# Performance work log

Measured on AMD Instinct MI355X. Metric: run time of the kernel, lower is better.

Reference implementation:

```python
import jax, jax.numpy as jnp
import numpy as np

NUM_CAPSULE = 16
DIM_CAPSULE = 64
ROUTINGS = 3
T_EPS = 1e-07


def squash(v, axis=-1):
    # NOTE: this repo's 'squash' is v / sqrt(||v||^2 + eps) (norm-only scaling)
    s = jnp.sum(v * v, axis=axis, keepdims=True)
    return v / jnp.sqrt(s + T_EPS)


def setup_inputs() -> dict:
    key = jax.random.key(0)
    k1, k2 = jax.random.split(key)
    B, N_in, D_in = 64, 512, 1024
    x = jax.random.normal(k1, (B, N_in, D_in), dtype=jnp.float32)
    # xavier-normal-ish init for W [1, D_in, num_capsule*dim_capsule]
    fan_in, fan_out = D_in, NUM_CAPSULE * DIM_CAPSULE
    std = float(np.sqrt(2.0 / (fan_in + fan_out)))
    W = jax.random.normal(k2, (1, D_in, NUM_CAPSULE * DIM_CAPSULE), dtype=jnp.float32) * std
    return {"x": x, "W": W}


def reference(x, W):
    B, N_in, D_in = x.shape
    # u_hat: [B, N_in, num_cap*dim_cap] -> [B, num_cap, N_in, dim_cap]
    u_hat = jnp.matmul(x, W[0])
    u_hat = u_hat.reshape(B, N_in, NUM_CAPSULE, DIM_CAPSULE).transpose(0, 2, 1, 3)
    b = jnp.zeros((B, NUM_CAPSULE, N_in), dtype=u_hat.dtype)
    outputs = None
    for i in range(ROUTINGS):
        # torch code permutes to [B, N_in, num_cap], softmaxes dim=2, permutes back:
        # equivalent to softmax over the num_capsule axis (axis=1)
        c = jax.nn.softmax(b, axis=1)  # [B, num_cap, N_in]
        outputs = squash(jnp.einsum('bij,bijk->bik', c, u_hat))  # [B, num_cap, dim_cap]
        if i < ROUTINGS - 1:
            b = jnp.einsum('bik,bijk->bij', outputs, u_hat)  # [B, num_cap, N_in]
    return outputs
```

## Files before the change

kernel.cpp:

```cpp
#include <hip/hip_runtime.h>
#include <stdint.h>

#define NUM_CAP 16
#define DIM_CAP 64
#define BATCH   64
#define N_IN    512
#define D_IN    1024
#define N_COL   1024
#define M_ROWS  (BATCH*N_IN)

typedef __attribute__((ext_vector_type(8))) short short8;
typedef __attribute__((ext_vector_type(4))) float f32x4;

__device__ __forceinline__ float bf2f(unsigned int u) {
  return __uint_as_float(u << 16);
}
__device__ __forceinline__ unsigned short f2bf_rne(float f) {
  unsigned int x = __float_as_uint(f);
  x += 0x7fffu + ((x >> 16) & 1u);
  return (unsigned short)(x >> 16);
}
__device__ __forceinline__ unsigned int pack_rne(unsigned int lo, unsigned int hi) {
  const unsigned int lr = lo + (0x7fffu + ((lo >> 16) & 1u));
  const unsigned int hr = hi + (0x7fffu + ((hi >> 16) & 1u));
  return (lr >> 16) | (hr & 0xffff0000u);
}

__global__ __launch_bounds__(256) void prep(
    const float* __restrict__ x, const float* __restrict__ W,
    unsigned short* __restrict__ xb, unsigned short* __restrict__ Wt) {
  const int t = threadIdx.x;
  if (blockIdx.x < 16384) {
    const size_t i = ((size_t)blockIdx.x * 256 + t) * 8;
    const uint4 a = *(const uint4*)(x + i);
    const uint4 b = *(const uint4*)(x + i + 4);
    uint4 p;
    p.x = pack_rne(a.x, a.y); p.y = pack_rne(a.z, a.w);
    p.z = pack_rne(b.x, b.y); p.w = pack_rne(b.z, b.w);
    *(uint4*)(xb + i) = p;
  } else {
    __shared__ float tile[32][33];
    const int bid = blockIdx.x - 16384;
    const int bx = bid & 31, by = bid >> 5;
    const int tx = t & 31, ty0 = t >> 5;
    #pragma unroll
    for (int r = 0; r < 4; r++) {
      const int ty = ty0 + r * 8;
      tile[ty][tx] = W[(size_t)(by * 32 + ty) * N_COL + bx * 32 + tx];
    }
    __syncthreads();
    #pragma unroll
    for (int r = 0; r < 4; r++) {
      const int ty = ty0 + r * 8;
      Wt[(size_t)(bx * 32 + ty) * D_IN + by * 32 + tx] = f2bf_rne(tile[tx][ty]);
    }
  }
}

__global__ __launch_bounds__(256) void gemm_uhat(
    const unsigned short* __restrict__ A,
    const unsigned short* __restrict__ Bt,
    unsigned short* __restrict__ C,
    float* __restrict__ Pp) {
  __shared__ __align__(16) unsigned short lA[128 * 32];
  __shared__ __align__(16) unsigned short lB[128 * 32];
  __shared__ float cs2[2][128];

  const int t = threadIdx.x;
  const int wave = t >> 6, lane = t & 63;
  const int xcd = blockIdx.x & 7, local = blockIdx.x >> 3;
  const int mt = xcd * 32 + (local >> 3), nt = local & 7;
  const int m0 = mt * 128, n0 = nt * 128;
  const int wm = wave & 1, wn = wave >> 1;

  f32x4 acc[4][4] = {};

  const int srow = lane >> 2;
  const int schunk = ((lane & 3) ^ ((srow >> 1) & 3)) * 8;

  for (int kt = 0; kt < D_IN / 32; ++kt) {
    const int k0 = kt * 32;
    __syncthreads();
    #pragma unroll
    for (int s0 = 0; s0 < 2; ++s0) {
      const int s = wave + s0 * 4;
      const unsigned short* ga = A + (size_t)(m0 + s * 16 + srow) * D_IN + k0 + schunk;
      __builtin_amdgcn_global_load_lds(
          (const __attribute__((address_space(1))) void*)ga,
          (__attribute__((address_space(3))) void*)(lA + s * 512), 16, 0, 0);
      const unsigned short* gb = Bt + (size_t)(n0 + s * 16 + srow) * D_IN + k0 + schunk;
      __builtin_amdgcn_global_load_lds(
          (const __attribute__((address_space(1))) void*)gb,
          (__attribute__((address_space(3))) void*)(lB + s * 512), 16, 0, 0);
    }
    __syncthreads();

    short8 af[4], bfr[4];
    const int rsel = lane & 15;
    const int q = lane >> 4;
    const int koff = (q ^ ((rsel >> 1) & 3)) * 8;
    #pragma unroll
    for (int tm = 0; tm < 4; tm++)
      af[tm] = *(const short8*)&lA[(wm * 64 + tm * 16 + rsel) * 32 + koff];
    #pragma unroll
    for (int tn = 0; tn < 4; tn++)
      bfr[tn] = *(const short8*)&lB[(wn * 64 + tn * 16 + rsel) * 32 + koff];
    #pragma unroll
    for (int tm = 0; tm < 4; tm++)
      #pragma unroll
      for (int tn = 0; tn < 4; tn++)
        acc[tm][tn] = __builtin_amdgcn_mfma_f32_16x16x32_bf16(
            af[tm], bfr[tn], acc[tm][tn], 0, 0, 0);
  }

  const int lrow = (lane >> 4) * 4, lcol = lane & 15;
  #pragma unroll
  for (int tm = 0; tm < 4; tm++)
    #pragma unroll
    for (int tn = 0; tn < 4; tn++)
      #pragma unroll
      for (int r = 0; r < 4; r++) {
        const int row = m0 + wm * 64 + tm * 16 + lrow + r;
        const int col = n0 + wn * 64 + tn * 16 + lcol;
        C[(size_t)row * N_COL + col] = f2bf_rne(acc[tm][tn][r]);
      }

  #pragma unroll
  for (int tn = 0; tn < 4; tn++) {
    float p = 0.f;
    #pragma unroll
    for (int tm = 0; tm < 4; tm++)
      #pragma unroll
      for (int r = 0; r < 4; r++) p += acc[tm][tn][r];
    p += __shfl_xor(p, 16);
    p += __shfl_xor(p, 32);
    if (lane < 16) cs2[wm][wn * 64 + tn * 16 + lane] = p;
  }
  __syncthreads();
  if (t < 128)
    Pp[(size_t)mt * N_COL + n0 + t] = cs2[0][t] + cs2[1][t];
}

__global__ __launch_bounds__(256) void k_v(
    const float* __restrict__ Pin, float* __restrict__ vout, const int nstrips) {
  const int b = blockIdx.x, t = threadIdx.x;
  float4 s = make_float4(0.f, 0.f, 0.f, 0.f);
  for (int q = 0; q < nstrips; ++q) {
    const float4 p = *(const float4*)&Pin[((size_t)b * nstrips + q) * 1024 + t * 4];
    s.x += p.x; s.y += p.y; s.z += p.z; s.w += p.w;
  }
  float ss = s.x * s.x + s.y * s.y + s.z * s.z + s.w * s.w;
  #pragma unroll
  for (int d = 1; d < 16; d <<= 1) ss += __shfl_xor(ss, d);
  const float inv = 1.f / sqrtf(ss + 1e-7f);
  *(float4*)&vout[(size_t)b * 1024 + t * 4] =
      make_float4(s.x * inv, s.y * inv, s.z * inv, s.w * inv);
}

__global__ __launch_bounds__(256) void route_mid(
    const unsigned short* __restrict__ uhat,
    const float* __restrict__ v,
    float* __restrict__ Pout) {
  __shared__ float sq[16 * 68];
  __shared__ float red[4][1024];
  const int t = threadIdx.x;
  const int w = t >> 6, lane = t & 63;
  const int b = blockIdx.x >> 5, jt = blockIdx.x & 31;
  const int i_l = lane >> 2, c4 = lane & 3;

  {
    const float4 vv = *(const float4*)&v[(size_t)b * 1024 + t * 4];
    *(float4*)&sq[(t >> 4) * 68 + (t & 15) * 4] = vv;
  }
  __syncthreads();

  float pv[16];
  #pragma unroll
  for (int q = 0; q < 4; q++)
    *(float4*)&pv[q * 4] = *(const float4*)&sq[i_l * 68 + c4 * 16 + q * 4];

  float acc[16];
  #pragma unroll
  for (int q = 0; q < 16; q++) acc[q] = 0.f;

  const unsigned short* ub =
      uhat + (size_t)(b * N_IN + jt * 16 + w * 4) * N_COL + lane * 16;

  uint4 c0 = *(const uint4*)ub;
  uint4 c1 = *(const uint4*)(ub + 8);
  #pragma unroll
  for (int jj = 0; jj < 4; ++jj) {
    uint4 n0v = c0, n1v = c1;
    if (jj < 3) {
      n0v = *(const uint4*)(ub + N_COL);
      n1v = *(const uint4*)(ub + N_COL + 8);
    }
    float u[16];
    #define UNP(wd, o) { u[(o)] = bf2f((wd) & 0xffffu); u[(o)+1] = __uint_as_float((wd) & 0xffff0000u); }
    UNP(c0.x, 0) UNP(c0.y, 2) UNP(c0.z, 4) UNP(c0.w, 6)
    UNP(c1.x, 8) UNP(c1.y, 10) UNP(c1.z, 12) UNP(c1.w, 14)
    #undef UNP

    float dot = 0.f;
    #pragma unroll
    for (int q = 0; q < 16; q++) dot = fmaf(pv[q], u[q], dot);
    dot += __shfl_xor(dot, 1);
    dot += __shfl_xor(dot, 2);
    const float e = __expf(dot);
    float s = e;
    #pragma unroll
    for (int d = 4; d < 64; d <<= 1) s += __shfl_xor(s, d);
    const float c = e / s;
    #pragma unroll
    for (int q = 0; q < 16; q++) acc[q] = fmaf(c, u[q], acc[q]);

    c0 = n0v; c1 = n1v; ub += N_COL;
  }

  #pragma unroll
  for (int q = 0; q < 4; q++)
    *(float4*)&red[w][lane * 16 + q * 4] = make_float4(
        acc[q * 4 + 0], acc[q * 4 + 1], acc[q * 4 + 2], acc[q * 4 + 3]);
  __syncthreads();
  float4 s4 = make_float4(0.f, 0.f, 0.f, 0.f);
  #pragma unroll
  for (int ww = 0; ww < 4; ++ww) {
    const float4 r = *(const float4*)&red[ww][t * 4];
    s4.x += r.x; s4.y += r.y; s4.z += r.z; s4.w += r.w;
  }
  *(float4*)&Pout[(size_t)blockIdx.x * 1024 + t * 4] = s4;
}

extern "C" void kernel_launch(void* const* d_in, const int* in_sizes, int n_in,
                              void* d_out, int out_size, void* d_ws, size_t ws_size,
                              hipStream_t stream) {
  const float* x = (const float*)d_in[0];
  const float* W = (const float*)d_in[1];
  float* out = (float*)d_out;

  char* ws = (char*)d_ws;
  unsigned short* Wt   = (unsigned short*)ws;
  unsigned short* uhat = (unsigned short*)(ws + (size_t)(2 << 20));
  float* Pp = (float*)(ws + (size_t)66 * (1 << 20));
  float* v1 = (float*)(ws + (size_t)67 * (1 << 20));
  float* v2 = (float*)(ws + (size_t)67 * (1 << 20) + (512 << 10));
  unsigned short* xb = (unsigned short*)(ws + (size_t)68 * (1 << 20));
  float* P1 = (float*)(ws + (size_t)68 * (1 << 20));
  float* P2 = (float*)(ws + (size_t)76 * (1 << 20));

  prep<<<16384 + 1024, 256, 0, stream>>>(x, W, xb, Wt);
  gemm_uhat<<<2048, 256, 0, stream>>>(xb, Wt, uhat, Pp);
  k_v<<<64, 256, 0, stream>>>(Pp, v1, 4);
  route_mid<<<2048, 256, 0, stream>>>(uhat, v1, P1);
  k_v<<<64, 256, 0, stream>>>(P1, v2, 32);
  route_mid<<<2048, 256, 0, stream>>>(uhat, v2, P2);
  k_v<<<64, 256, 0, stream>>>(P2, out, 32);
}
```

Measured before the change: 335.9 us.

## Fuse squash reduction into routing kernel, remap blocks per XCD, batch uhat loads

The k_v squash kernels are removed. Every route_mid block now sums the partial strips itself and normalizes v, which saves two launches and the v round trip through memory. Block indices are remapped so that each XCD handles contiguous batches, which should improve L2 locality of the uhat reads. All four uhat rows are loaded up front instead of double-buffered, and a wider k_out kernel handles the final reduction. The trade-off is redundant work: each of the 32 blocks per batch re-reads up to 32 strips to rebuild v, and the extra live loads raise register pressure.

```diff
diff --git a/kernel.cpp b/kernel.cpp
--- a/kernel.cpp
+++ b/kernel.cpp
@@ -141,37 +141,31 @@
     Pp[(size_t)mt * N_COL + n0 + t] = cs2[0][t] + cs2[1][t];
 }
 
-__global__ __launch_bounds__(256) void k_v(
-    const float* __restrict__ Pin, float* __restrict__ vout, const int nstrips) {
-  const int b = blockIdx.x, t = threadIdx.x;
-  float4 s = make_float4(0.f, 0.f, 0.f, 0.f);
-  for (int q = 0; q < nstrips; ++q) {
-    const float4 p = *(const float4*)&Pin[((size_t)b * nstrips + q) * 1024 + t * 4];
-    s.x += p.x; s.y += p.y; s.z += p.z; s.w += p.w;
-  }
-  float ss = s.x * s.x + s.y * s.y + s.z * s.z + s.w * s.w;
+__global__ __launch_bounds__(256) void route_mid(
+    const unsigned short* __restrict__ uhat,
+    const float* __restrict__ Vin,
+    float* __restrict__ Pout,
+    const int nstrips) {
+  __shared__ float sq[16 * 68];
+  __shared__ float red[4][1024];
+  const int t = threadIdx.x;
+  const int w = t >> 6, lane = t & 63;
+  const int xcd = blockIdx.x & 7, kk = blockIdx.x >> 3;
+  const int b = xcd * 8 + (kk >> 5), jt = kk & 31;
+  const int tid = b * 32 + jt;
+  const int i_l = lane >> 2, c4 = lane & 3;
+
+  float4 v4 = make_float4(0.f, 0.f, 0.f, 0.f);
+  for (int s = 0; s < nstrips; ++s) {
+    const float4 ps = *(const float4*)&Vin[((size_t)b * nstrips + s) * 1024 + t * 4];
+    v4.x += ps.x; v4.y += ps.y; v4.z += ps.z; v4.w += ps.w;
+  }
+  float ss = v4.x * v4.x + v4.y * v4.y + v4.z * v4.z + v4.w * v4.w;
   #pragma unroll
   for (int d = 1; d < 16; d <<= 1) ss += __shfl_xor(ss, d);
   const float inv = 1.f / sqrtf(ss + 1e-7f);
-  *(float4*)&vout[(size_t)b * 1024 + t * 4] =
-      make_float4(s.x * inv, s.y * inv, s.z * inv, s.w * inv);
-}
-
-__global__ __launch_bounds__(256) void route_mid(
-    const unsigned short* __restrict__ uhat,
-    const float* __restrict__ v,
-    float* __restrict__ Pout) {
-  __shared__ float sq[16 * 68];
-  __shared__ float red[4][1024];
-  const int t = threadIdx.x;
-  const int w = t >> 6, lane = t & 63;
-  const int b = blockIdx.x >> 5, jt = blockIdx.x & 31;
-  const int i_l = lane >> 2, c4 = lane & 3;
-
-  {
-    const float4 vv = *(const float4*)&v[(size_t)b * 1024 + t * 4];
-    *(float4*)&sq[(t >> 4) * 68 + (t & 15) * 4] = vv;
-  }
+  *(float4*)&sq[(t >> 4) * 68 + (t & 15) * 4] =
+      make_float4(v4.x * inv, v4.y * inv, v4.z * inv, v4.w * inv);
   __syncthreads();
 
   float pv[16];
@@ -186,19 +180,19 @@
   const unsigned short* ub =
       uhat + (size_t)(b * N_IN + jt * 16 + w * 4) * N_COL + lane * 16;
 
-  uint4 c0 = *(const uint4*)ub;
-  uint4 c1 = *(const uint4*)(ub + 8);
+  uint4 d0[4], d1[4];
   #pragma unroll
   for (int jj = 0; jj < 4; ++jj) {
-    uint4 n0v = c0, n1v = c1;
-    if (jj < 3) {
-      n0v = *(const uint4*)(ub + N_COL);
-      n1v = *(const uint4*)(ub + N_COL + 8);
-    }
+    d0[jj] = *(const uint4*)(ub + (size_t)jj * N_COL);
+    d1[jj] = *(const uint4*)(ub + (size_t)jj * N_COL + 8);
+  }
+
+  #pragma unroll
+  for (int jj = 0; jj < 4; ++jj) {
     float u[16];
     #define UNP(wd, o) { u[(o)] = bf2f((wd) & 0xffffu); u[(o)+1] = __uint_as_float((wd) & 0xffff0000u); }
-    UNP(c0.x, 0) UNP(c0.y, 2) UNP(c0.z, 4) UNP(c0.w, 6)
-    UNP(c1.x, 8) UNP(c1.y, 10) UNP(c1.z, 12) UNP(c1.w, 14)
+    UNP(d0[jj].x, 0) UNP(d0[jj].y, 2) UNP(d0[jj].z, 4) UNP(d0[jj].w, 6)
+    UNP(d1[jj].x, 8) UNP(d1[jj].y, 10) UNP(d1[jj].z, 12) UNP(d1[jj].w, 14)
     #undef UNP
 
     float dot = 0.f;
@@ -213,8 +207,6 @@
     const float c = e / s;
     #pragma unroll
     for (int q = 0; q < 16; q++) acc[q] = fmaf(c, u[q], acc[q]);
-
-    c0 = n0v; c1 = n1v; ub += N_COL;
   }
 
   #pragma unroll
@@ -228,7 +220,22 @@
     const float4 r = *(const float4*)&red[ww][t * 4];
     s4.x += r.x; s4.y += r.y; s4.z += r.z; s4.w += r.w;
   }
-  *(float4*)&Pout[(size_t)blockIdx.x * 1024 + t * 4] = s4;
+  *(float4*)&Pout[(size_t)tid * 1024 + t * 4] = s4;
+}
+
+__global__ __launch_bounds__(256) void k_out(
+    const float* __restrict__ P, float* __restrict__ out) {
+  const int b = blockIdx.x >> 2, ic = blockIdx.x & 3;
+  const int t = threadIdx.x;
+  const int i = ic * 4 + (t >> 6), k = t & 63;
+  const float* p = P + (size_t)b * 32 * 1024 + i * 64 + k;
+  float s = 0.f;
+  #pragma unroll
+  for (int q = 0; q < 32; ++q) s += p[(size_t)q * 1024];
+  float ss = s * s;
+  #pragma unroll
+  for (int d = 1; d < 64; d <<= 1) ss += __shfl_xor(ss, d);
+  out[((size_t)b * 16 + i) * 64 + k] = s / sqrtf(ss + 1e-7f);
 }
 
 extern "C" void kernel_launch(void* const* d_in, const int* in_sizes, int n_in,
@@ -242,17 +249,13 @@
   unsigned short* Wt   = (unsigned short*)ws;
   unsigned short* uhat = (unsigned short*)(ws + (size_t)(2 << 20));
   float* Pp = (float*)(ws + (size_t)66 * (1 << 20));
-  float* v1 = (float*)(ws + (size_t)67 * (1 << 20));
-  float* v2 = (float*)(ws + (size_t)67 * (1 << 20) + (512 << 10));
   unsigned short* xb = (unsigned short*)(ws + (size_t)68 * (1 << 20));
   float* P1 = (float*)(ws + (size_t)68 * (1 << 20));
   float* P2 = (float*)(ws + (size_t)76 * (1 << 20));
 
   prep<<<16384 + 1024, 256, 0, stream>>>(x, W, xb, Wt);
   gemm_uhat<<<2048, 256, 0, stream>>>(xb, Wt, uhat, Pp);
-  k_v<<<64, 256, 0, stream>>>(Pp, v1, 4);
-  route_mid<<<2048, 256, 0, stream>>>(uhat, v1, P1);
-  k_v<<<64, 256, 0, stream>>>(P1, v2, 32);
-  route_mid<<<2048, 256, 0, stream>>>(uhat, v2, P2);
-  k_v<<<64, 256, 0, stream>>>(P2, out, 32);
-}
+  route_mid<<<2048, 256, 0, stream>>>(uhat, Pp, P1, 4);
+  route_mid<<<2048, 256, 0, stream>>>(uhat, P1, P2, 32);
+  k_out<<<256, 256, 0, stream>>>(P2, out);
+}
```

Result: no change. 335.2 us (-0.2%).
